# Kernel tuning notes

Measured on AMD Instinct MI355X. Metric: run time of the kernel, lower is better.

The kernel has to match this reference:

```python
import jax, jax.numpy as jnp
import numpy as np

INPUT, HIDDEN, PROJ = 4, 64, 49
B, T = 2048, 512


def setup_inputs() -> dict:
    key = jax.random.key(0)
    ks = jax.random.split(key, 8)
    s = 1.0 / np.sqrt(HIDDEN)
    u = lambda k, shape: jax.random.uniform(k, shape, jnp.float32, -s, s)
    return {
        "x": jax.random.normal(ks[0], (B, T, INPUT), jnp.float32),
        "W_ih": u(ks[1], (4 * HIDDEN, INPUT)),   # gates order i,f,g,o
        "W_hh": u(ks[2], (4 * HIDDEN, PROJ)),    # recurrent input is projected h (size PROJ)
        "b_ih": u(ks[3], (4 * HIDDEN,)),
        "b_hh": u(ks[4], (4 * HIDDEN,)),
        "W_hr": u(ks[5], (PROJ, HIDDEN)),        # projection h_full -> h
        "W_out": u(ks[6], (PROJ, PROJ)),         # final linear on last projected hidden state
        "b_out": u(ks[7], (PROJ,)),
    }


def reference(x, W_ih, W_hh, b_ih, b_hh, W_hr, W_out, b_out):
    Bx = x.shape[0]
    # precompute input contribution for all timesteps: [B, T, 4H]
    x_gates = jnp.einsum('bti,gi->btg', x, W_ih) + b_ih + b_hh

    def step(carry, xg_t):
        h, c = carry                      # h: [B, PROJ], c: [B, HIDDEN]
        gates = xg_t + h @ W_hh.T         # [B, 4H]
        i, f, g, o = jnp.split(gates, 4, axis=-1)
        i = jax.nn.sigmoid(i)
        f = jax.nn.sigmoid(f)
        g = jnp.tanh(g)
        o = jax.nn.sigmoid(o)
        c = f * c + i * g
        h_full = o * jnp.tanh(c)          # [B, HIDDEN]
        h = h_full @ W_hr.T               # [B, PROJ]
        return (h, c), None

    h0 = jnp.zeros((Bx, PROJ), x.dtype)
    c0 = jnp.zeros((Bx, HIDDEN), x.dtype)
    (h_last, _), _ = jax.lax.scan(step, (h0, c0), jnp.swapaxes(x_gates, 0, 1))
    return h_last @ W_out.T + b_out       # [B, PROJ]
```

## Files before the change

### kernel.cpp

```cpp
#include <hip/hip_runtime.h>

#define TSTEPS 512
#define BPB    4
#define ROWB   256
#define ABYTES (16 * ROWB)
#define KSTEPS 3

typedef short bf16x8 __attribute__((ext_vector_type(8)));
typedef float f32x4  __attribute__((ext_vector_type(4)));

__device__ __forceinline__ float fast_sigmoid(float x) {
    return __builtin_amdgcn_rcpf(1.0f + __expf(-x));
}
__device__ __forceinline__ float fast_tanh(float x) {
    return 1.0f - 2.0f * __builtin_amdgcn_rcpf(__expf(2.0f * x) + 1.0f);
}
__device__ __forceinline__ unsigned int f2bf(float f) {
    unsigned int u = __builtin_bit_cast(unsigned int, f);
    return (u + 0x7FFFu + ((u >> 16) & 1u)) >> 16;
}
__device__ __forceinline__ float bf2f(unsigned int us) {
    return __builtin_bit_cast(float, us << 16);
}
__device__ __forceinline__ unsigned int split_pack(float f) {
    unsigned int hi = f2bf(f);
    unsigned int lo = f2bf(f - bf2f(hi));
    return hi | (lo << 16);
}

__global__ __launch_bounds__(256, 2) void lstm_mfma5_kernel(
    const float* __restrict__ x,
    const float* __restrict__ W_ih,
    const float* __restrict__ W_hh,
    const float* __restrict__ b_ih,
    const float* __restrict__ b_hh,
    const float* __restrict__ W_hr,
    const float* __restrict__ W_out,
    const float* __restrict__ b_out,
    float* __restrict__ out)
{
    const int tid = threadIdx.x;
    const int w   = tid >> 6;
    const int l   = tid & 63;
    const int g4  = l >> 4;
    const int ln  = l & 15;
    const int b0  = blockIdx.x * BPB;

    __shared__ __align__(128) unsigned char Abuf[2 * ABYTES];
    __shared__ __align__(16)  float hf32[BPB][64];
    __shared__ float hproj[BPB][52];

    for (int i = tid; i < (2 * ABYTES) / 4; i += 256)
        ((unsigned int*)Abuf)[i] = 0u;
    __syncthreads();

    float Msum[4][16];
    #pragma unroll
    for (int t4 = 0; t4 < 4; ++t4)
        #pragma unroll
        for (int i = 0; i < 16; ++i) Msum[t4][i] = 0.0f;

    for (int p = 0; p < 49; ++p) {
        float wr[16];
        #pragma unroll
        for (int s = 0; s < 2; ++s)
            #pragma unroll
            for (int j = 0; j < 8; ++j)
                wr[s * 8 + j] = W_hr[p * 64 + s * 32 + g4 * 8 + j];
        #pragma unroll
        for (int t4 = 0; t4 < 4; ++t4) {
            const float whh = W_hh[(t4 * 64 + w * 16 + ln) * 49 + p];
            #pragma unroll
            for (int i = 0; i < 16; ++i) Msum[t4][i] += whh * wr[i];
        }
    }

    bf16x8 Bf[4][KSTEPS];
    union U { unsigned int d[4]; bf16x8 v; };
    #pragma unroll
    for (int t4 = 0; t4 < 4; ++t4) {
        #pragma unroll
        for (int s = 0; s < 2; ++s) {
            U u;
            #pragma unroll
            for (int jj = 0; jj < 4; ++jj) {
                const unsigned int e0 = f2bf(Msum[t4][s * 8 + 2 * jj]);
                const unsigned int e1 = f2bf(Msum[t4][s * 8 + 2 * jj + 1]);
                u.d[jj] = e0 | (e1 << 16);
            }
            Bf[t4][s] = u.v;
        }
        U u; u.d[0] = u.d[1] = u.d[2] = u.d[3] = 0u;
        const int n = t4 * 64 + w * 16 + ln;
        if (g4 == 0) {
            #pragma unroll
            for (int c = 0; c < 4; ++c) {
                const unsigned int us = f2bf(W_ih[n * 4 + c]);
                u.d[c] = us | (us << 16);
            }
        } else if (g4 == 1) {
            u.d[0] = f2bf(b_ih[n] + b_hh[n]);
        }
        Bf[t4][2] = u.v;
    }

    const bool xduty = ((tid & 15) == 0);
    int xbase = 0, xrowbyte = 0;
    float xw = 0.f, xn = 0.f;
    if (xduty) {
        const int v    = tid >> 4;
        const int bl   = v >> 2;
        const int comp = v & 3;
        const int row  = bl * 4;
        xbase    = (b0 + bl) * (TSTEPS * 4) + comp;
        xrowbyte = (row * ROWB + 128 + 4 * comp) ^ ((row & 7) << 4);
        *(unsigned int*)(Abuf + xrowbyte) = split_pack(x[xbase]);
        xw = x[xbase + 4 * 1];
        xn = x[xbase + 4 * 2];
    }
    if (tid < 32) {
        const int row = tid & 15, buf = tid >> 4;
        const int byte = (row * ROWB + 144) ^ ((row & 7) << 4);
        *(unsigned int*)(Abuf + buf * ABYTES + byte) = 0x3F80u;
    }
    __syncthreads();

    int aoff[KSTEPS];
    #pragma unroll
    for (int s = 0; s < KSTEPS; ++s)
        aoff[s] = (ln * ROWB + s * 64 + g4 * 16) ^ ((ln & 7) << 4);
    const int wrow  = g4 * 4;
    const int woff0 = (wrow * ROWB + 2 * (w * 16 + ln)) ^ ((wrow & 7) << 4);

    float cst = 0.f;
    float hffin = 0.f;
    int cur = 0;

    for (int t = 0; t < TSTEPS; ++t) {
        float xn2 = 0.0f;
        if (xduty) {
            const int tt = (t + 3 < TSTEPS) ? t + 3 : TSTEPS - 1;
            xn2 = x[xbase + 4 * tt];
        }

        const unsigned char* Ab = Abuf + cur * ABYTES;
        bf16x8 af[KSTEPS];
        #pragma unroll
        for (int s = 0; s < KSTEPS; ++s)
            af[s] = *(const bf16x8*)(Ab + aoff[s]);

        f32x4 aI = {0.f, 0.f, 0.f, 0.f}, aF = aI, aG = aI, aO = aI;
        #pragma unroll
        for (int s = 0; s < KSTEPS; ++s) {
            aI = __builtin_amdgcn_mfma_f32_16x16x32_bf16(af[s], Bf[0][s], aI, 0, 0, 0);
            aF = __builtin_amdgcn_mfma_f32_16x16x32_bf16(af[s], Bf[1][s], aF, 0, 0, 0);
            aG = __builtin_amdgcn_mfma_f32_16x16x32_bf16(af[s], Bf[2][s], aG, 0, 0, 0);
            aO = __builtin_amdgcn_mfma_f32_16x16x32_bf16(af[s], Bf[3][s], aO, 0, 0, 0);
        }

        unsigned char* An = Abuf + (cur ^ 1) * ABYTES;
        {
            const float gi = fast_sigmoid(aI[0]);
            const float gf = fast_sigmoid(aF[0]);
            const float gg = fast_tanh(aG[0]);
            const float go = fast_sigmoid(aO[0]);
            cst = gf * cst + gi * gg;
            const float hf = go * fast_tanh(cst);
            hffin = hf;
            *(unsigned short*)(An + woff0) = (unsigned short)f2bf(hf);
        }
        if (xduty)
            *(unsigned int*)(An + xrowbyte) = split_pack(xw);
        xw = xn; xn = xn2;

        __syncthreads();
        cur ^= 1;
    }

    hf32[g4][w * 16 + ln] = hffin;
    __syncthreads();

    for (int idx = tid; idx < BPB * 49; idx += 256) {
        const int bb = idx / 49, q = idx - bb * 49;
        float s = 0.0f;
        #pragma unroll 8
        for (int h = 0; h < 64; ++h) s += hf32[bb][h] * W_hr[q * 64 + h];
        hproj[bb][q] = s;
    }
    __syncthreads();
    for (int idx = tid; idx < BPB * 49; idx += 256) {
        const int bb = idx / 49, q2 = idx - bb * 49;
        float s = b_out[q2];
        #pragma unroll 7
        for (int p = 0; p < 49; ++p) s += hproj[bb][p] * W_out[q2 * 49 + p];
        out[(b0 + bb) * 49 + q2] = s;
    }
}

extern "C" void kernel_launch(void* const* d_in, const int* in_sizes, int n_in,
                              void* d_out, int out_size, void* d_ws, size_t ws_size,
                              hipStream_t stream) {
    (void)in_sizes; (void)n_in; (void)d_ws; (void)ws_size; (void)out_size;
    const float* x     = (const float*)d_in[0];
    const float* W_ih  = (const float*)d_in[1];
    const float* W_hh  = (const float*)d_in[2];
    const float* b_ih  = (const float*)d_in[3];
    const float* b_hh  = (const float*)d_in[4];
    const float* W_hr  = (const float*)d_in[5];
    const float* W_out = (const float*)d_in[6];
    const float* b_out = (const float*)d_in[7];
    float* outp = (float*)d_out;

    lstm_mfma5_kernel<<<dim3(2048 / BPB), dim3(256), 0, stream>>>(
        x, W_ih, W_hh, b_ih, b_hh, W_hr, W_out, b_out, outp);
}
```

Baseline: 224.0 us.

## Move input projection out of MFMA into per-lane FP32 FMAs with LDS-staged x

Drops the third MFMA k-step, which carried the split-bf16 x values and the bias, and instead computes the W_ih·x + bias contribution per lane in FP32 from register-held weights. x is bulk-loaded every 64 steps into a shared-memory staging buffer with float4 loads, replacing the per-step scalar prefetch pipeline. The hidden-state write is packed into 32-bit stores via a lane shuffle. This cuts MFMA count and LDS A-reads per step, at the cost of an extra barrier every 64 steps and more VALU work per step.

```diff
diff --git a/kernel.cpp b/kernel.cpp
--- a/kernel.cpp
+++ b/kernel.cpp
@@ -4,7 +4,7 @@
 #define BPB    4
 #define ROWB   256
 #define ABYTES (16 * ROWB)
-#define KSTEPS 3
+#define KSTEPS 2
 
 typedef short bf16x8 __attribute__((ext_vector_type(8)));
 typedef float f32x4  __attribute__((ext_vector_type(4)));
@@ -19,16 +19,8 @@
     unsigned int u = __builtin_bit_cast(unsigned int, f);
     return (u + 0x7FFFu + ((u >> 16) & 1u)) >> 16;
 }
-__device__ __forceinline__ float bf2f(unsigned int us) {
-    return __builtin_bit_cast(float, us << 16);
-}
-__device__ __forceinline__ unsigned int split_pack(float f) {
-    unsigned int hi = f2bf(f);
-    unsigned int lo = f2bf(f - bf2f(hi));
-    return hi | (lo << 16);
-}
 
-__global__ __launch_bounds__(256, 2) void lstm_mfma5_kernel(
+__global__ __launch_bounds__(256, 2) void lstm_mfma6_kernel(
     const float* __restrict__ x,
     const float* __restrict__ W_ih,
     const float* __restrict__ W_hh,
@@ -47,12 +39,12 @@
     const int b0  = blockIdx.x * BPB;
 
     __shared__ __align__(128) unsigned char Abuf[2 * ABYTES];
+    __shared__ __align__(128) unsigned char Xreg[64 * 64];
     __shared__ __align__(16)  float hf32[BPB][64];
     __shared__ float hproj[BPB][52];
 
     for (int i = tid; i < (2 * ABYTES) / 4; i += 256)
         ((unsigned int*)Abuf)[i] = 0u;
-    __syncthreads();
 
     float Msum[4][16];
     #pragma unroll
@@ -90,88 +82,76 @@
             }
             Bf[t4][s] = u.v;
         }
-        U u; u.d[0] = u.d[1] = u.d[2] = u.d[3] = 0u;
-        const int n = t4 * 64 + w * 16 + ln;
-        if (g4 == 0) {
-            #pragma unroll
-            for (int c = 0; c < 4; ++c) {
-                const unsigned int us = f2bf(W_ih[n * 4 + c]);
-                u.d[c] = us | (us << 16);
-            }
-        } else if (g4 == 1) {
-            u.d[0] = f2bf(b_ih[n] + b_hh[n]);
-        }
-        Bf[t4][2] = u.v;
     }
 
-    const bool xduty = ((tid & 15) == 0);
-    int xbase = 0, xrowbyte = 0;
-    float xw = 0.f, xn = 0.f;
-    if (xduty) {
-        const int v    = tid >> 4;
-        const int bl   = v >> 2;
-        const int comp = v & 3;
-        const int row  = bl * 4;
-        xbase    = (b0 + bl) * (TSTEPS * 4) + comp;
-        xrowbyte = (row * ROWB + 128 + 4 * comp) ^ ((row & 7) << 4);
-        *(unsigned int*)(Abuf + xrowbyte) = split_pack(x[xbase]);
-        xw = x[xbase + 4 * 1];
-        xn = x[xbase + 4 * 2];
+    float wih[4][4], bsum[4];
+    #pragma unroll
+    for (int t4 = 0; t4 < 4; ++t4) {
+        const int n = t4 * 64 + w * 16 + ln;
+        #pragma unroll
+        for (int c = 0; c < 4; ++c) wih[t4][c] = W_ih[n * 4 + c];
+        bsum[t4] = b_ih[n] + b_hh[n];
     }
-    if (tid < 32) {
-        const int row = tid & 15, buf = tid >> 4;
-        const int byte = (row * ROWB + 144) ^ ((row & 7) << 4);
-        *(unsigned int*)(Abuf + buf * ABYTES + byte) = 0x3F80u;
-    }
-    __syncthreads();
 
     int aoff[KSTEPS];
     #pragma unroll
     for (int s = 0; s < KSTEPS; ++s)
         aoff[s] = (ln * ROWB + s * 64 + g4 * 16) ^ ((ln & 7) << 4);
     const int wrow  = g4 * 4;
-    const int woff0 = (wrow * ROWB + 2 * (w * 16 + ln)) ^ ((wrow & 7) << 4);
+    const int woffp = (wrow * ROWB + 2 * (w * 16 + ln)) ^ ((wrow & 7) << 4);
 
     float cst = 0.f;
     float hffin = 0.f;
     int cur = 0;
+    __syncthreads();
 
     for (int t = 0; t < TSTEPS; ++t) {
-        float xn2 = 0.0f;
-        if (xduty) {
-            const int tt = (t + 3 < TSTEPS) ? t + 3 : TSTEPS - 1;
-            xn2 = x[xbase + 4 * tt];
+        if ((t & 63) == 0) {
+            const float4 xv = *reinterpret_cast<const float4*>(
+                x + ((size_t)(b0 + w) * TSTEPS + (t + l)) * 4);
+            *reinterpret_cast<float4*>(Xreg + l * 64 + w * 16) = xv;
+            __syncthreads();
         }
 
         const unsigned char* Ab = Abuf + cur * ABYTES;
-        bf16x8 af[KSTEPS];
-        #pragma unroll
-        for (int s = 0; s < KSTEPS; ++s)
-            af[s] = *(const bf16x8*)(Ab + aoff[s]);
+        const bf16x8 af0 = *(const bf16x8*)(Ab + aoff[0]);
+        const bf16x8 af1 = *(const bf16x8*)(Ab + aoff[1]);
+        const float4 xt = *reinterpret_cast<const float4*>(
+            Xreg + ((t & 63) << 6) + (g4 << 4));
 
         f32x4 aI = {0.f, 0.f, 0.f, 0.f}, aF = aI, aG = aI, aO = aI;
-        #pragma unroll
-        for (int s = 0; s < KSTEPS; ++s) {
-            aI = __builtin_amdgcn_mfma_f32_16x16x32_bf16(af[s], Bf[0][s], aI, 0, 0, 0);
-            aF = __builtin_amdgcn_mfma_f32_16x16x32_bf16(af[s], Bf[1][s], aF, 0, 0, 0);
-            aG = __builtin_amdgcn_mfma_f32_16x16x32_bf16(af[s], Bf[2][s], aG, 0, 0, 0);
-            aO = __builtin_amdgcn_mfma_f32_16x16x32_bf16(af[s], Bf[3][s], aO, 0, 0, 0);
-        }
+        aI = __builtin_amdgcn_mfma_f32_16x16x32_bf16(af0, Bf[0][0], aI, 0, 0, 0);
+        aF = __builtin_amdgcn_mfma_f32_16x16x32_bf16(af0, Bf[1][0], aF, 0, 0, 0);
+        aG = __builtin_amdgcn_mfma_f32_16x16x32_bf16(af0, Bf[2][0], aG, 0, 0, 0);
+        aO = __builtin_amdgcn_mfma_f32_16x16x32_bf16(af0, Bf[3][0], aO, 0, 0, 0);
+        aI = __builtin_amdgcn_mfma_f32_16x16x32_bf16(af1, Bf[0][1], aI, 0, 0, 0);
+        aF = __builtin_amdgcn_mfma_f32_16x16x32_bf16(af1, Bf[1][1], aF, 0, 0, 0);
+        aG = __builtin_amdgcn_mfma_f32_16x16x32_bf16(af1, Bf[2][1], aG, 0, 0, 0);
+        aO = __builtin_amdgcn_mfma_f32_16x16x32_bf16(af1, Bf[3][1], aO, 0, 0, 0);
+
+        const float xgI = fmaf(wih[0][3], xt.w, fmaf(wih[0][2], xt.z,
+                          fmaf(wih[0][1], xt.y, fmaf(wih[0][0], xt.x, bsum[0]))));
+        const float xgF = fmaf(wih[1][3], xt.w, fmaf(wih[1][2], xt.z,
+                          fmaf(wih[1][1], xt.y, fmaf(wih[1][0], xt.x, bsum[1]))));
+        const float xgG = fmaf(wih[2][3], xt.w, fmaf(wih[2][2], xt.z,
+                          fmaf(wih[2][1], xt.y, fmaf(wih[2][0], xt.x, bsum[2]))));
+        const float xgO = fmaf(wih[3][3], xt.w, fmaf(wih[3][2], xt.z,
+                          fmaf(wih[3][1], xt.y, fmaf(wih[3][0], xt.x, bsum[3]))));
 
         unsigned char* An = Abuf + (cur ^ 1) * ABYTES;
         {
-            const float gi = fast_sigmoid(aI[0]);
-            const float gf = fast_sigmoid(aF[0]);
-            const float gg = fast_tanh(aG[0]);
-            const float go = fast_sigmoid(aO[0]);
+            const float gi = fast_sigmoid(aI[0] + xgI);
+            const float gf = fast_sigmoid(aF[0] + xgF);
+            const float gg = fast_tanh(aG[0] + xgG);
+            const float go = fast_sigmoid(aO[0] + xgO);
             cst = gf * cst + gi * gg;
             const float hf = go * fast_tanh(cst);
             hffin = hf;
-            *(unsigned short*)(An + woff0) = (unsigned short)f2bf(hf);
+            const unsigned int ub = f2bf(hf);
+            const unsigned int up = __shfl_xor(ub, 1);
+            if (!(ln & 1))
+                *(unsigned int*)(An + woffp) = ub | (up << 16);
         }
-        if (xduty)
-            *(unsigned int*)(An + xrowbyte) = split_pack(xw);
-        xw = xn; xn = xn2;
 
         __syncthreads();
         cur ^= 1;
@@ -211,6 +191,6 @@
     const float* b_out = (const float*)d_in[7];
     float* outp = (float*)d_out;
 
-    lstm_mfma5_kernel<<<dim3(2048 / BPB), dim3(256), 0, stream>>>(
+    lstm_mfma6_kernel<<<dim3(2048 / BPB), dim3(256), 0, stream>>>(
         x, W_ih, W_hh, b_ih, b_hh, W_hr, W_out, b_out, outp);
 }
```

New measurement: 239.4 us. +6.8%, slower.

## Split gate MFMAs across two wave groups with LDS exchange, 8 sequences per block

Applied to the files above, without the earlier changes.

Doubles the block to 512 threads and 8 batch rows. Each half of the waves now computes two of the four gate tiles, using two rows of the 16-row MFMA A tile instead of one. The gate pre-activations are swapped through shared memory with an extra barrier per timestep. The -log2e / 2·log2e scaling is folded into the bf16 weights so the activations use raw exp2 plus rcp, and the h stores are packed in pairs via a lane shuffle. The aim is to halve the serial MFMA chain per wave and cut transcendental ALU work, at the cost of a second __syncthreads per step and fewer blocks overall.

```diff
diff --git a/kernel.cpp b/kernel.cpp
--- a/kernel.cpp
+++ b/kernel.cpp
@@ -1,20 +1,14 @@
 #include <hip/hip_runtime.h>
 
 #define TSTEPS 512
-#define BPB    4
+#define BPB    8
 #define ROWB   256
 #define ABYTES (16 * ROWB)
-#define KSTEPS 3
+#define LOG2E  1.44269504088896340736f
 
 typedef short bf16x8 __attribute__((ext_vector_type(8)));
 typedef float f32x4  __attribute__((ext_vector_type(4)));
 
-__device__ __forceinline__ float fast_sigmoid(float x) {
-    return __builtin_amdgcn_rcpf(1.0f + __expf(-x));
-}
-__device__ __forceinline__ float fast_tanh(float x) {
-    return 1.0f - 2.0f * __builtin_amdgcn_rcpf(__expf(2.0f * x) + 1.0f);
-}
 __device__ __forceinline__ unsigned int f2bf(float f) {
     unsigned int u = __builtin_bit_cast(unsigned int, f);
     return (u + 0x7FFFu + ((u >> 16) & 1u)) >> 16;
@@ -27,8 +21,11 @@
     unsigned int lo = f2bf(f - bf2f(hi));
     return hi | (lo << 16);
 }
-
-__global__ __launch_bounds__(256, 2) void lstm_mfma5_kernel(
+__device__ __forceinline__ float rcp1p(float e) {
+    return __builtin_amdgcn_rcpf(1.0f + e);
+}
+
+__global__ __launch_bounds__(512, 2) void lstm_mfma8_kernel(
     const float* __restrict__ x,
     const float* __restrict__ W_ih,
     const float* __restrict__ W_hh,
@@ -41,67 +38,72 @@
 {
     const int tid = threadIdx.x;
     const int w   = tid >> 6;
+    const int p   = w >> 2;
+    const int c   = w & 3;
     const int l   = tid & 63;
     const int g4  = l >> 4;
     const int ln  = l & 15;
     const int b0  = blockIdx.x * BPB;
 
     __shared__ __align__(128) unsigned char Abuf[2 * ABYTES];
-    __shared__ __align__(16)  float hf32[BPB][64];
+    __shared__ float ex[2 * 4 * 2 * 64];
+    __shared__ __align__(16) float hf32[BPB][64];
     __shared__ float hproj[BPB][52];
 
-    for (int i = tid; i < (2 * ABYTES) / 4; i += 256)
+    for (int i = tid; i < (2 * ABYTES) / 4; i += 512)
         ((unsigned int*)Abuf)[i] = 0u;
-    __syncthreads();
-
-    float Msum[4][16];
+
+    float Msum[2][16];
     #pragma unroll
-    for (int t4 = 0; t4 < 4; ++t4)
-        #pragma unroll
-        for (int i = 0; i < 16; ++i) Msum[t4][i] = 0.0f;
-
-    for (int p = 0; p < 49; ++p) {
+    for (int i = 0; i < 2; ++i)
+        #pragma unroll
+        for (int k = 0; k < 16; ++k) Msum[i][k] = 0.0f;
+
+    for (int q = 0; q < 49; ++q) {
         float wr[16];
         #pragma unroll
         for (int s = 0; s < 2; ++s)
             #pragma unroll
             for (int j = 0; j < 8; ++j)
-                wr[s * 8 + j] = W_hr[p * 64 + s * 32 + g4 * 8 + j];
-        #pragma unroll
-        for (int t4 = 0; t4 < 4; ++t4) {
-            const float whh = W_hh[(t4 * 64 + w * 16 + ln) * 49 + p];
-            #pragma unroll
-            for (int i = 0; i < 16; ++i) Msum[t4][i] += whh * wr[i];
-        }
-    }
-
-    bf16x8 Bf[4][KSTEPS];
+                wr[s * 8 + j] = W_hr[q * 64 + s * 32 + g4 * 8 + j];
+        #pragma unroll
+        for (int i = 0; i < 2; ++i) {
+            const int n = (2 * p + i) * 64 + c * 16 + ln;
+            const float whh = W_hh[n * 49 + q];
+            #pragma unroll
+            for (int k = 0; k < 16; ++k) Msum[i][k] += whh * wr[k];
+        }
+    }
+
+    bf16x8 Bf[2][3];
     union U { unsigned int d[4]; bf16x8 v; };
     #pragma unroll
-    for (int t4 = 0; t4 < 4; ++t4) {
+    for (int i = 0; i < 2; ++i) {
+        const int t4 = 2 * p + i;
+        const float fac = (t4 == 2) ? 2.0f * LOG2E : -LOG2E;
         #pragma unroll
         for (int s = 0; s < 2; ++s) {
             U u;
             #pragma unroll
             for (int jj = 0; jj < 4; ++jj) {
-                const unsigned int e0 = f2bf(Msum[t4][s * 8 + 2 * jj]);
-                const unsigned int e1 = f2bf(Msum[t4][s * 8 + 2 * jj + 1]);
+                const unsigned int e0 = f2bf(fac * Msum[i][s * 8 + 2 * jj]);
+                const unsigned int e1 = f2bf(fac * Msum[i][s * 8 + 2 * jj + 1]);
                 u.d[jj] = e0 | (e1 << 16);
             }
-            Bf[t4][s] = u.v;
+            Bf[i][s] = u.v;
         }
         U u; u.d[0] = u.d[1] = u.d[2] = u.d[3] = 0u;
-        const int n = t4 * 64 + w * 16 + ln;
+        const int n = t4 * 64 + c * 16 + ln;
         if (g4 == 0) {
             #pragma unroll
-            for (int c = 0; c < 4; ++c) {
-                const unsigned int us = f2bf(W_ih[n * 4 + c]);
-                u.d[c] = us | (us << 16);
+            for (int c4 = 0; c4 < 4; ++c4) {
+                const unsigned int us = f2bf(fac * W_ih[n * 4 + c4]);
+                u.d[c4] = us | (us << 16);
             }
         } else if (g4 == 1) {
-            u.d[0] = f2bf(b_ih[n] + b_hh[n]);
-        }
-        Bf[t4][2] = u.v;
+            u.d[0] = f2bf(fac * (b_ih[n] + b_hh[n]));
+        }
+        Bf[i][2] = u.v;
     }
 
     const bool xduty = ((tid & 15) == 0);
@@ -111,7 +113,7 @@
         const int v    = tid >> 4;
         const int bl   = v >> 2;
         const int comp = v & 3;
-        const int row  = bl * 4;
+        const int row  = ((bl & 6) << 1) | (bl & 1);
         xbase    = (b0 + bl) * (TSTEPS * 4) + comp;
         xrowbyte = (row * ROWB + 128 + 4 * comp) ^ ((row & 7) << 4);
         *(unsigned int*)(Abuf + xrowbyte) = split_pack(x[xbase]);
@@ -125,15 +127,16 @@
     }
     __syncthreads();
 
-    int aoff[KSTEPS];
+    int aoff[3];
     #pragma unroll
-    for (int s = 0; s < KSTEPS; ++s)
+    for (int s = 0; s < 3; ++s)
         aoff[s] = (ln * ROWB + s * 64 + g4 * 16) ^ ((ln & 7) << 4);
-    const int wrow  = g4 * 4;
-    const int woff0 = (wrow * ROWB + 2 * (w * 16 + ln)) ^ ((wrow & 7) << 4);
-
-    float cst = 0.f;
-    float hffin = 0.f;
+    const int wrow  = g4 * 4 + p;
+    const int woffp = (wrow * ROWB + 2 * (c * 16 + ln)) ^ ((wrow & 7) << 4);
+    const int exw   = ((p * 4 + c) * 2) * 64 + l;
+    const int exr   = (((1 - p) * 4 + c) * 2) * 64 + l;
+
+    float cst = 0.f, hffin = 0.f;
     int cur = 0;
 
     for (int t = 0; t < TSTEPS; ++t) {
@@ -144,31 +147,44 @@
         }
 
         const unsigned char* Ab = Abuf + cur * ABYTES;
-        bf16x8 af[KSTEPS];
-        #pragma unroll
-        for (int s = 0; s < KSTEPS; ++s)
-            af[s] = *(const bf16x8*)(Ab + aoff[s]);
-
-        f32x4 aI = {0.f, 0.f, 0.f, 0.f}, aF = aI, aG = aI, aO = aI;
-        #pragma unroll
-        for (int s = 0; s < KSTEPS; ++s) {
-            aI = __builtin_amdgcn_mfma_f32_16x16x32_bf16(af[s], Bf[0][s], aI, 0, 0, 0);
-            aF = __builtin_amdgcn_mfma_f32_16x16x32_bf16(af[s], Bf[1][s], aF, 0, 0, 0);
-            aG = __builtin_amdgcn_mfma_f32_16x16x32_bf16(af[s], Bf[2][s], aG, 0, 0, 0);
-            aO = __builtin_amdgcn_mfma_f32_16x16x32_bf16(af[s], Bf[3][s], aO, 0, 0, 0);
-        }
+        const bf16x8 af0 = *(const bf16x8*)(Ab + aoff[0]);
+        const bf16x8 af1 = *(const bf16x8*)(Ab + aoff[1]);
+        const bf16x8 af2 = *(const bf16x8*)(Ab + aoff[2]);
+
+        f32x4 accA = {0.f, 0.f, 0.f, 0.f}, accB = accA;
+        accA = __builtin_amdgcn_mfma_f32_16x16x32_bf16(af0, Bf[0][0], accA, 0, 0, 0);
+        accB = __builtin_amdgcn_mfma_f32_16x16x32_bf16(af0, Bf[1][0], accB, 0, 0, 0);
+        accA = __builtin_amdgcn_mfma_f32_16x16x32_bf16(af1, Bf[0][1], accA, 0, 0, 0);
+        accB = __builtin_amdgcn_mfma_f32_16x16x32_bf16(af1, Bf[1][1], accB, 0, 0, 0);
+        accA = __builtin_amdgcn_mfma_f32_16x16x32_bf16(af2, Bf[0][2], accA, 0, 0, 0);
+        accB = __builtin_amdgcn_mfma_f32_16x16x32_bf16(af2, Bf[1][2], accB, 0, 0, 0);
+
+        ex[exw]      = accA[1 - p];
+        ex[exw + 64] = accB[1 - p];
+        __syncthreads();
+        const float rA = ex[exr];
+        const float rB = ex[exr + 64];
+
+        float aIv, aFv, aGv, aOv;
+        if (p == 0) { aIv = accA[0]; aFv = accB[0]; aGv = rA;      aOv = rB;      }
+        else        { aGv = accA[1]; aOv = accB[1]; aIv = rA;      aFv = rB;      }
+
+        const float gi = rcp1p(__builtin_amdgcn_exp2f(aIv));
+        const float gf = rcp1p(__builtin_amdgcn_exp2f(aFv));
+        const float rg = rcp1p(__builtin_amdgcn_exp2f(aGv));
+        const float gg = fmaf(-2.0f, rg, 1.0f);
+        const float go = rcp1p(__builtin_amdgcn_exp2f(aOv));
+        cst = fmaf(gf, cst, gi * gg);
+        const float rc = rcp1p(__builtin_amdgcn_exp2f(cst * (2.0f * LOG2E)));
+        const float th = fmaf(-2.0f, rc, 1.0f);
+        const float hf = go * th;
+        hffin = hf;
 
         unsigned char* An = Abuf + (cur ^ 1) * ABYTES;
-        {
-            const float gi = fast_sigmoid(aI[0]);
-            const float gf = fast_sigmoid(aF[0]);
-            const float gg = fast_tanh(aG[0]);
-            const float go = fast_sigmoid(aO[0]);
-            cst = gf * cst + gi * gg;
-            const float hf = go * fast_tanh(cst);
-            hffin = hf;
-            *(unsigned short*)(An + woff0) = (unsigned short)f2bf(hf);
-        }
+        const unsigned int ub = f2bf(hf);
+        const unsigned int up = __shfl_xor(ub, 1);
+        if (!(ln & 1))
+            *(unsigned int*)(An + woffp) = ub | (up << 16);
         if (xduty)
             *(unsigned int*)(An + xrowbyte) = split_pack(xw);
         xw = xn; xn = xn2;
@@ -177,10 +193,10 @@
         cur ^= 1;
     }
 
-    hf32[g4][w * 16 + ln] = hffin;
+    hf32[g4 * 2 + p][c * 16 + ln] = hffin;
     __syncthreads();
 
-    for (int idx = tid; idx < BPB * 49; idx += 256) {
+    for (int idx = tid; idx < BPB * 49; idx += 512) {
         const int bb = idx / 49, q = idx - bb * 49;
         float s = 0.0f;
         #pragma unroll 8
@@ -188,11 +204,11 @@
         hproj[bb][q] = s;
     }
     __syncthreads();
-    for (int idx = tid; idx < BPB * 49; idx += 256) {
+    for (int idx = tid; idx < BPB * 49; idx += 512) {
         const int bb = idx / 49, q2 = idx - bb * 49;
         float s = b_out[q2];
         #pragma unroll 7
-        for (int p = 0; p < 49; ++p) s += hproj[bb][p] * W_out[q2 * 49 + p];
+        for (int q = 0; q < 49; ++q) s += hproj[bb][q] * W_out[q2 * 49 + q];
         out[(b0 + bb) * 49 + q2] = s;
     }
 }
@@ -211,6 +227,6 @@
     const float* b_out = (const float*)d_in[7];
     float* outp = (float*)d_out;
 
-    lstm_mfma5_kernel<<<dim3(2048 / BPB), dim3(256), 0, stream>>>(
+    lstm_mfma8_kernel<<<dim3(2048 / BPB), dim3(512), 0, stream>>>(
         x, W_ih, W_hh, b_ih, b_hh, W_hr, W_out, b_out, outp);
 }
```

Measured after the change: 315.4 us. 40.8% more time.

## Interleave two independent batch chains per block and fold exp scaling into weights

Applied to the files above, without the earlier changes.

Each block now handles 8 batch rows as two independent recurrence chains (A and B), with separate double-buffered LDS tiles, so one chain's MFMA and activation work can overlap the other's latency within a single barrier per step. The gate weights and biases are pre-scaled by -log2e (or 2·log2e for the g gate) so activations use exp2 directly without an extra multiply. The hidden-state LDS store is packed into 32-bit writes via a lane shuffle. Grid size halves to 256 blocks and occupancy hint drops to 1 block per CU, which risks leaving CUs underused. Pre-scaling before bf16 rounding also changes the numerics slightly.

```diff
diff --git a/kernel.cpp b/kernel.cpp
--- a/kernel.cpp
+++ b/kernel.cpp
@@ -1,20 +1,14 @@
 #include <hip/hip_runtime.h>
 
 #define TSTEPS 512
-#define BPB    4
+#define BPB    8
 #define ROWB   256
 #define ABYTES (16 * ROWB)
-#define KSTEPS 3
+#define LOG2E  1.44269504088896340736f
 
 typedef short bf16x8 __attribute__((ext_vector_type(8)));
 typedef float f32x4  __attribute__((ext_vector_type(4)));
 
-__device__ __forceinline__ float fast_sigmoid(float x) {
-    return __builtin_amdgcn_rcpf(1.0f + __expf(-x));
-}
-__device__ __forceinline__ float fast_tanh(float x) {
-    return 1.0f - 2.0f * __builtin_amdgcn_rcpf(__expf(2.0f * x) + 1.0f);
-}
 __device__ __forceinline__ unsigned int f2bf(float f) {
     unsigned int u = __builtin_bit_cast(unsigned int, f);
     return (u + 0x7FFFu + ((u >> 16) & 1u)) >> 16;
@@ -27,8 +21,11 @@
     unsigned int lo = f2bf(f - bf2f(hi));
     return hi | (lo << 16);
 }
-
-__global__ __launch_bounds__(256, 2) void lstm_mfma5_kernel(
+__device__ __forceinline__ float rcp1p(float e) {
+    return __builtin_amdgcn_rcpf(1.0f + e);
+}
+
+__global__ __launch_bounds__(256, 1) void lstm_mfma9_kernel(
     const float* __restrict__ x,
     const float* __restrict__ W_ih,
     const float* __restrict__ W_hh,
@@ -46,13 +43,12 @@
     const int ln  = l & 15;
     const int b0  = blockIdx.x * BPB;
 
-    __shared__ __align__(128) unsigned char Abuf[2 * ABYTES];
+    __shared__ __align__(128) unsigned char Abuf[4 * ABYTES];
     __shared__ __align__(16)  float hf32[BPB][64];
     __shared__ float hproj[BPB][52];
 
-    for (int i = tid; i < (2 * ABYTES) / 4; i += 256)
+    for (int i = tid; i < (4 * ABYTES) / 4; i += 256)
         ((unsigned int*)Abuf)[i] = 0u;
-    __syncthreads();
 
     float Msum[4][16];
     #pragma unroll
@@ -60,32 +56,33 @@
         #pragma unroll
         for (int i = 0; i < 16; ++i) Msum[t4][i] = 0.0f;
 
-    for (int p = 0; p < 49; ++p) {
+    for (int q = 0; q < 49; ++q) {
         float wr[16];
         #pragma unroll
         for (int s = 0; s < 2; ++s)
             #pragma unroll
             for (int j = 0; j < 8; ++j)
-                wr[s * 8 + j] = W_hr[p * 64 + s * 32 + g4 * 8 + j];
+                wr[s * 8 + j] = W_hr[q * 64 + s * 32 + g4 * 8 + j];
         #pragma unroll
         for (int t4 = 0; t4 < 4; ++t4) {
-            const float whh = W_hh[(t4 * 64 + w * 16 + ln) * 49 + p];
+            const float whh = W_hh[(t4 * 64 + w * 16 + ln) * 49 + q];
             #pragma unroll
             for (int i = 0; i < 16; ++i) Msum[t4][i] += whh * wr[i];
         }
     }
 
-    bf16x8 Bf[4][KSTEPS];
+    bf16x8 Bf[4][3];
     union U { unsigned int d[4]; bf16x8 v; };
     #pragma unroll
     for (int t4 = 0; t4 < 4; ++t4) {
+        const float fac = (t4 == 2) ? 2.0f * LOG2E : -LOG2E;
         #pragma unroll
         for (int s = 0; s < 2; ++s) {
             U u;
             #pragma unroll
             for (int jj = 0; jj < 4; ++jj) {
-                const unsigned int e0 = f2bf(Msum[t4][s * 8 + 2 * jj]);
-                const unsigned int e1 = f2bf(Msum[t4][s * 8 + 2 * jj + 1]);
+                const unsigned int e0 = f2bf(fac * Msum[t4][s * 8 + 2 * jj]);
+                const unsigned int e1 = f2bf(fac * Msum[t4][s * 8 + 2 * jj + 1]);
                 u.d[jj] = e0 | (e1 << 16);
             }
             Bf[t4][s] = u.v;
@@ -94,46 +91,47 @@
         const int n = t4 * 64 + w * 16 + ln;
         if (g4 == 0) {
             #pragma unroll
-            for (int c = 0; c < 4; ++c) {
-                const unsigned int us = f2bf(W_ih[n * 4 + c]);
-                u.d[c] = us | (us << 16);
+            for (int c4 = 0; c4 < 4; ++c4) {
+                const unsigned int us = f2bf(fac * W_ih[n * 4 + c4]);
+                u.d[c4] = us | (us << 16);
             }
         } else if (g4 == 1) {
-            u.d[0] = f2bf(b_ih[n] + b_hh[n]);
+            u.d[0] = f2bf(fac * (b_ih[n] + b_hh[n]));
         }
         Bf[t4][2] = u.v;
     }
 
-    const bool xduty = ((tid & 15) == 0);
+    const bool xduty = ((tid & 7) == 0);
     int xbase = 0, xrowbyte = 0;
     float xw = 0.f, xn = 0.f;
     if (xduty) {
-        const int v    = tid >> 4;
-        const int bl   = v >> 2;
-        const int comp = v & 3;
-        const int row  = bl * 4;
+        const int v     = tid >> 3;
+        const int bl    = v >> 2;
+        const int comp  = v & 3;
+        const int chain = bl >> 2;
+        const int row   = (bl & 3) * 4;
         xbase    = (b0 + bl) * (TSTEPS * 4) + comp;
-        xrowbyte = (row * ROWB + 128 + 4 * comp) ^ ((row & 7) << 4);
+        xrowbyte = chain * 2 * ABYTES +
+                   ((row * ROWB + 128 + 4 * comp) ^ ((row & 7) << 4));
         *(unsigned int*)(Abuf + xrowbyte) = split_pack(x[xbase]);
         xw = x[xbase + 4 * 1];
         xn = x[xbase + 4 * 2];
     }
-    if (tid < 32) {
+    if (tid < 64) {
         const int row = tid & 15, buf = tid >> 4;
         const int byte = (row * ROWB + 144) ^ ((row & 7) << 4);
         *(unsigned int*)(Abuf + buf * ABYTES + byte) = 0x3F80u;
     }
     __syncthreads();
 
-    int aoff[KSTEPS];
+    int aoff[3];
     #pragma unroll
-    for (int s = 0; s < KSTEPS; ++s)
+    for (int s = 0; s < 3; ++s)
         aoff[s] = (ln * ROWB + s * 64 + g4 * 16) ^ ((ln & 7) << 4);
     const int wrow  = g4 * 4;
-    const int woff0 = (wrow * ROWB + 2 * (w * 16 + ln)) ^ ((wrow & 7) << 4);
-
-    float cst = 0.f;
-    float hffin = 0.f;
+    const int woffp = (wrow * ROWB + 2 * (w * 16 + ln)) ^ ((wrow & 7) << 4);
+
+    float cstA = 0.f, cstB = 0.f, hffinA = 0.f, hffinB = 0.f;
     int cur = 0;
 
     for (int t = 0; t < TSTEPS; ++t) {
@@ -143,41 +141,84 @@
             xn2 = x[xbase + 4 * tt];
         }
 
-        const unsigned char* Ab = Abuf + cur * ABYTES;
-        bf16x8 af[KSTEPS];
-        #pragma unroll
-        for (int s = 0; s < KSTEPS; ++s)
-            af[s] = *(const bf16x8*)(Ab + aoff[s]);
-
-        f32x4 aI = {0.f, 0.f, 0.f, 0.f}, aF = aI, aG = aI, aO = aI;
-        #pragma unroll
-        for (int s = 0; s < KSTEPS; ++s) {
-            aI = __builtin_amdgcn_mfma_f32_16x16x32_bf16(af[s], Bf[0][s], aI, 0, 0, 0);
-            aF = __builtin_amdgcn_mfma_f32_16x16x32_bf16(af[s], Bf[1][s], aF, 0, 0, 0);
-            aG = __builtin_amdgcn_mfma_f32_16x16x32_bf16(af[s], Bf[2][s], aG, 0, 0, 0);
-            aO = __builtin_amdgcn_mfma_f32_16x16x32_bf16(af[s], Bf[3][s], aO, 0, 0, 0);
-        }
-
-        unsigned char* An = Abuf + (cur ^ 1) * ABYTES;
+        const unsigned char* Aa = Abuf + cur * ABYTES;
+        const unsigned char* Ab = Abuf + 2 * ABYTES + cur * ABYTES;
+        const bf16x8 a0 = *(const bf16x8*)(Aa + aoff[0]);
+        const bf16x8 a1 = *(const bf16x8*)(Aa + aoff[1]);
+        const bf16x8 a2 = *(const bf16x8*)(Aa + aoff[2]);
+        const bf16x8 b0f = *(const bf16x8*)(Ab + aoff[0]);
+        const bf16x8 b1f = *(const bf16x8*)(Ab + aoff[1]);
+        const bf16x8 b2f = *(const bf16x8*)(Ab + aoff[2]);
+
+        f32x4 AI = {0.f,0.f,0.f,0.f}, AF = AI, AG = AI, AO = AI;
+        f32x4 BI = AI, BF_ = AI, BG = AI, BO = AI;
+        AI = __builtin_amdgcn_mfma_f32_16x16x32_bf16(a0, Bf[0][0], AI, 0, 0, 0);
+        AF = __builtin_amdgcn_mfma_f32_16x16x32_bf16(a0, Bf[1][0], AF, 0, 0, 0);
+        AG = __builtin_amdgcn_mfma_f32_16x16x32_bf16(a0, Bf[2][0], AG, 0, 0, 0);
+        AO = __builtin_amdgcn_mfma_f32_16x16x32_bf16(a0, Bf[3][0], AO, 0, 0, 0);
+        AI = __builtin_amdgcn_mfma_f32_16x16x32_bf16(a1, Bf[0][1], AI, 0, 0, 0);
+        AF = __builtin_amdgcn_mfma_f32_16x16x32_bf16(a1, Bf[1][1], AF, 0, 0, 0);
+        AG = __builtin_amdgcn_mfma_f32_16x16x32_bf16(a1, Bf[2][1], AG, 0, 0, 0);
+        AO = __builtin_amdgcn_mfma_f32_16x16x32_bf16(a1, Bf[3][1], AO, 0, 0, 0);
+        AI = __builtin_amdgcn_mfma_f32_16x16x32_bf16(a2, Bf[0][2], AI, 0, 0, 0);
+        AF = __builtin_amdgcn_mfma_f32_16x16x32_bf16(a2, Bf[1][2], AF, 0, 0, 0);
+        AG = __builtin_amdgcn_mfma_f32_16x16x32_bf16(a2, Bf[2][2], AG, 0, 0, 0);
+        AO = __builtin_amdgcn_mfma_f32_16x16x32_bf16(a2, Bf[3][2], AO, 0, 0, 0);
+        BI = __builtin_amdgcn_mfma_f32_16x16x32_bf16(b0f, Bf[0][0], BI, 0, 0, 0);
+        BF_= __builtin_amdgcn_mfma_f32_16x16x32_bf16(b0f, Bf[1][0], BF_, 0, 0, 0);
+        BG = __builtin_amdgcn_mfma_f32_16x16x32_bf16(b0f, Bf[2][0], BG, 0, 0, 0);
+        BO = __builtin_amdgcn_mfma_f32_16x16x32_bf16(b0f, Bf[3][0], BO, 0, 0, 0);
+        BI = __builtin_amdgcn_mfma_f32_16x16x32_bf16(b1f, Bf[0][1], BI, 0, 0, 0);
+        BF_= __builtin_amdgcn_mfma_f32_16x16x32_bf16(b1f, Bf[1][1], BF_, 0, 0, 0);
+        BG = __builtin_amdgcn_mfma_f32_16x16x32_bf16(b1f, Bf[2][1], BG, 0, 0, 0);
+        BO = __builtin_amdgcn_mfma_f32_16x16x32_bf16(b1f, Bf[3][1], BO, 0, 0, 0);
+        BI = __builtin_amdgcn_mfma_f32_16x16x32_bf16(b2f, Bf[0][2], BI, 0, 0, 0);
+        BF_= __builtin_amdgcn_mfma_f32_16x16x32_bf16(b2f, Bf[1][2], BF_, 0, 0, 0);
+        BG = __builtin_amdgcn_mfma_f32_16x16x32_bf16(b2f, Bf[2][2], BG, 0, 0, 0);
+        BO = __builtin_amdgcn_mfma_f32_16x16x32_bf16(b2f, Bf[3][2], BO, 0, 0, 0);
+
+        unsigned char* NA = Abuf + (cur ^ 1) * ABYTES;
+        unsigned char* NB = Abuf + 2 * ABYTES + (cur ^ 1) * ABYTES;
         {
-            const float gi = fast_sigmoid(aI[0]);
-            const float gf = fast_sigmoid(aF[0]);
-            const float gg = fast_tanh(aG[0]);
-            const float go = fast_sigmoid(aO[0]);
-            cst = gf * cst + gi * gg;
-            const float hf = go * fast_tanh(cst);
-            hffin = hf;
-            *(unsigned short*)(An + woff0) = (unsigned short)f2bf(hf);
+            const float gi = rcp1p(__builtin_amdgcn_exp2f(AI[0]));
+            const float gf = rcp1p(__builtin_amdgcn_exp2f(AF[0]));
+            const float rg = rcp1p(__builtin_amdgcn_exp2f(AG[0]));
+            const float gg = fmaf(-2.0f, rg, 1.0f);
+            const float go = rcp1p(__builtin_amdgcn_exp2f(AO[0]));
+            cstA = fmaf(gf, cstA, gi * gg);
+            const float rc = rcp1p(__builtin_amdgcn_exp2f(cstA * (2.0f * LOG2E)));
+            const float hf = go * fmaf(-2.0f, rc, 1.0f);
+            hffinA = hf;
+            const unsigned int ub = f2bf(hf);
+            const unsigned int up = __shfl_xor(ub, 1);
+            if (!(ln & 1))
+                *(unsigned int*)(NA + woffp) = ub | (up << 16);
+        }
+        {
+            const float gi = rcp1p(__builtin_amdgcn_exp2f(BI[0]));
+            const float gf = rcp1p(__builtin_amdgcn_exp2f(BF_[0]));
+            const float rg = rcp1p(__builtin_amdgcn_exp2f(BG[0]));
+            const float gg = fmaf(-2.0f, rg, 1.0f);
+            const float go = rcp1p(__builtin_amdgcn_exp2f(BO[0]));
+            cstB = fmaf(gf, cstB, gi * gg);
+            const float rc = rcp1p(__builtin_amdgcn_exp2f(cstB * (2.0f * LOG2E)));
+            const float hf = go * fmaf(-2.0f, rc, 1.0f);
+            hffinB = hf;
+            const unsigned int ub = f2bf(hf);
+            const unsigned int up = __shfl_xor(ub, 1);
+            if (!(ln & 1))
+                *(unsigned int*)(NB + woffp) = ub | (up << 16);
         }
         if (xduty)
-            *(unsigned int*)(An + xrowbyte) = split_pack(xw);
+            *(unsigned int*)(Abuf + (cur ^ 1) * ABYTES + xrowbyte) = split_pack(xw);
         xw = xn; xn = xn2;
 
         __syncthreads();
         cur ^= 1;
     }
 
-    hf32[g4][w * 16 + ln] = hffin;
+    hf32[g4][w * 16 + ln]     = hffinA;
+    hf32[4 + g4][w * 16 + ln] = hffinB;
     __syncthreads();
 
     for (int idx = tid; idx < BPB * 49; idx += 256) {
@@ -211,6 +252,6 @@
     const float* b_out = (const float*)d_in[7];
     float* outp = (float*)d_out;
 
-    lstm_mfma5_kernel<<<dim3(2048 / BPB), dim3(256), 0, stream>>>(
+    lstm_mfma9_kernel<<<dim3(2048 / BPB), dim3(256), 0, stream>>>(
         x, W_ih, W_hh, b_ih, b_hh, W_hr, W_out, b_out, outp);
 }
```

Result: slower. 310.1 us (+38.4%).
